# Kernel optimization log

Measured on AMD Instinct MI355X. Metric: run time of the kernel, lower is better.

Reference implementation:

```python
import jax, jax.numpy as jnp
import numpy as np

EPS = 1e-05
NEG = -1000000000.0

def rmsnorm(x):
    var = jnp.mean(x * x, axis=-1, keepdims=True)
    return x * jax.lax.rsqrt(var + EPS)

def apply_rotary(x, cos, sin):
    # x: [B,T,H,D], cos/sin: [T,D]
    d = x.shape[-1]
    x1, x2 = x[..., : d // 2], x[..., d // 2 :]
    half_rot = jnp.concatenate([-x2, x1], axis=-1)
    c = cos[None, :, None, :]
    s = sin[None, :, None, :]
    return x * c + half_rot * s

def setup_inputs() -> dict:
    key = jax.random.key(0)
    ks = jax.random.split(key, 12)
    B, T, C, H = 2, 2048, 1024, 16
    hd = C // H
    std = 0.02
    return {
        "x": jax.random.normal(ks[0], (B, T, C), jnp.float32),
        "x0": jax.random.normal(ks[1], (B, T, C), jnp.float32),
        "lambdaResid": jnp.ones((), jnp.float32),
        "lambdaX0": jnp.ones((), jnp.float32),
        "cos": jax.random.uniform(ks[2], (T, hd), jnp.float32),
        "sin": jax.random.uniform(ks[3], (T, hd), jnp.float32),
        "qWeight": jax.random.normal(ks[4], (C, C), jnp.float32) * std,
        "kWeight": jax.random.normal(ks[5], (C, C), jnp.float32) * std,
        "vWeight": jax.random.normal(ks[6], (C, C), jnp.float32) * std,
        "projWeight": jax.random.normal(ks[7], (C, C), jnp.float32) * std,
        "fcWeight": jax.random.normal(ks[8], (C, 4 * C), jnp.float32) * std,
        "mlpProjWeight": jax.random.normal(ks[9], (4 * C, C), jnp.float32) * std,
    }

def reference(x, x0, lambdaResid, lambdaX0, cos, sin,
              qWeight, kWeight, vWeight, projWeight, fcWeight, mlpProjWeight):
    B, T, C = x.shape
    hd = cos.shape[-1]
    H = C // hd
    scaled = x * lambdaResid + x0 * lambdaX0
    pre = rmsnorm(scaled)
    q = (pre @ qWeight).reshape(B, T, H, hd)
    k = (pre @ kWeight).reshape(B, T, H, hd)
    v = (pre @ vWeight).reshape(B, T, H, hd)
    q = rmsnorm(apply_rotary(q, cos, sin))  # [B,T,H,D]
    k = rmsnorm(apply_rotary(k, cos, sin))
    scores = jnp.einsum('bthd,bshd->bhts', q, k) / jnp.sqrt(jnp.float32(hd))
    mask = jnp.tril(jnp.ones((T, T), bool))
    scores = jnp.where(mask[None, None], scores, NEG)
    probs = jax.nn.softmax(scores, axis=-1)
    attn = jnp.einsum('bhts,bshd->bthd', probs, v).reshape(B, T, C)
    scaled = scaled + attn @ projWeight
    h = rmsnorm(scaled) @ fcWeight
    h = jnp.square(jax.nn.relu(h))
    return scaled + h @ mlpProjWeight
```

## Files before the change

kernel.cpp:

```cpp
#include <hip/hip_runtime.h>
#include <hip/hip_bf16.h>
#include <stdint.h>

typedef _Float16 f16;
typedef __attribute__((ext_vector_type(8))) _Float16 f16x8;
typedef __attribute__((ext_vector_type(4))) _Float16 f16x4;
typedef __attribute__((ext_vector_type(2))) __fp16 fp16x2;
typedef __attribute__((ext_vector_type(4))) float f32x4;

__device__ __forceinline__ void g2l16(const void* g, void* l) {
  __builtin_amdgcn_global_load_lds(
      (const __attribute__((address_space(1))) uint32_t*)g,
      (__attribute__((address_space(3))) uint32_t*)l, 16, 0, 0);
}

__device__ __forceinline__ uint32_t pkrtz(float a, float b) {
  union { fp16x2 h; uint32_t u; } z;
  z.h = __builtin_amdgcn_cvt_pkrtz(a, b);
  return z.u;
}

__global__ __launch_bounds__(256)
void wconv_all_kernel(const float* __restrict__ Wq, const float* __restrict__ Wk,
                      const float* __restrict__ Wv, const float* __restrict__ Wp,
                      const float* __restrict__ Wfc, const float* __restrict__ Wmp,
                      f16* __restrict__ Dq, f16* __restrict__ Dk, f16* __restrict__ Dv,
                      f16* __restrict__ Dp, f16* __restrict__ Dfc, f16* __restrict__ Dmp)
{
  __shared__ float tile[32][33];
  int id = blockIdx.x;
  const float* W; f16* Wt; int K, N, local;
  if      (id < 1024) { W = Wq;  Wt = Dq;  K = 1024; N = 1024; local = id; }
  else if (id < 2048) { W = Wk;  Wt = Dk;  K = 1024; N = 1024; local = id - 1024; }
  else if (id < 3072) { W = Wv;  Wt = Dv;  K = 1024; N = 1024; local = id - 2048; }
  else if (id < 4096) { W = Wp;  Wt = Dp;  K = 1024; N = 1024; local = id - 3072; }
  else if (id < 8192) { W = Wfc; Wt = Dfc; K = 1024; N = 4096; local = id - 4096; }
  else                { W = Wmp; Wt = Dmp; K = 4096; N = 1024; local = id - 8192; }
  int ntx = N >> 5;
  int n0 = (local % ntx) * 32, k0 = (local / ntx) * 32;
  int tx = threadIdx.x & 31, ty = threadIdx.x >> 5;
#pragma unroll
  for (int i = 0; i < 4; ++i)
    tile[ty + 8*i][tx] = W[(size_t)(k0 + ty + 8*i) * N + (n0 + tx)];
  __syncthreads();
#pragma unroll
  for (int i = 0; i < 4; ++i)
    Wt[(size_t)(n0 + ty + 8*i) * K + (k0 + tx)] = (f16)tile[tx][ty + 8*i];
}

__global__ __launch_bounds__(256)
void scale_rms_kernel(const float* __restrict__ x, const float* __restrict__ x0,
                      const float* __restrict__ lamR, const float* __restrict__ lamX,
                      float* __restrict__ scaled, f16* __restrict__ pre)
{
  const int C = 1024;
  int row = blockIdx.x, tid = threadIdx.x;
  float lr = lamR[0], lx = lamX[0];
  size_t base = (size_t)row * C;
  float4 xv = ((const float4*)(x + base))[tid];
  float4 zv = ((const float4*)(x0 + base))[tid];
  float4 sv;
  sv.x = xv.x*lr + zv.x*lx;  sv.y = xv.y*lr + zv.y*lx;
  sv.z = xv.z*lr + zv.z*lx;  sv.w = xv.w*lr + zv.w*lx;
  float ss = sv.x*sv.x + sv.y*sv.y + sv.z*sv.z + sv.w*sv.w;
#pragma unroll
  for (int off = 32; off >= 1; off >>= 1) ss += __shfl_xor(ss, off);
  __shared__ float red[4];
  if ((tid & 63) == 0) red[tid >> 6] = ss;
  __syncthreads();
  float tot = red[0] + red[1] + red[2] + red[3];
  float rs = rsqrtf(tot * (1.0f / 1024.0f) + 1e-5f);
  ((float4*)(scaled + base))[tid] = sv;
  f16* p = pre + base + tid * 4;
  p[0] = (f16)(sv.x * rs); p[1] = (f16)(sv.y * rs);
  p[2] = (f16)(sv.z * rs); p[3] = (f16)(sv.w * rs);
}

__global__ __launch_bounds__(256)
void combine_rms_kernel(const float* __restrict__ resid, const f16* __restrict__ p0,
                        const f16* __restrict__ p1, float* __restrict__ scaled2,
                        f16* __restrict__ pre2)
{
  const int C = 1024;
  int row = blockIdx.x, tid = threadIdx.x;
  size_t base = (size_t)row * C;
  float4 rv = ((const float4*)(resid + base))[tid];
  f16x4 av = ((const f16x4*)(p0 + base))[tid];
  f16x4 bv = ((const f16x4*)(p1 + base))[tid];
  float4 sv;
  sv.x = rv.x + (float)av[0] + (float)bv[0];
  sv.y = rv.y + (float)av[1] + (float)bv[1];
  sv.z = rv.z + (float)av[2] + (float)bv[2];
  sv.w = rv.w + (float)av[3] + (float)bv[3];
  float ss = sv.x*sv.x + sv.y*sv.y + sv.z*sv.z + sv.w*sv.w;
#pragma unroll
  for (int off = 32; off >= 1; off >>= 1) ss += __shfl_xor(ss, off);
  __shared__ float red[4];
  if ((tid & 63) == 0) red[tid >> 6] = ss;
  __syncthreads();
  float tot = red[0] + red[1] + red[2] + red[3];
  float rs = rsqrtf(tot * (1.0f / 1024.0f) + 1e-5f);
  ((float4*)(scaled2 + base))[tid] = sv;
  f16* p = pre2 + base + tid * 4;
  p[0] = (f16)(sv.x * rs); p[1] = (f16)(sv.y * rs);
  p[2] = (f16)(sv.z * rs); p[3] = (f16)(sv.w * rs);
}

__global__ __launch_bounds__(256)
void combine_out4_kernel(const float* __restrict__ resid, const f16* __restrict__ parts,
                         size_t pstride, float* __restrict__ out)
{
  size_t i = (size_t)blockIdx.x * 256 + threadIdx.x;
  float4 rv = ((const float4*)resid)[i];
  float4 sv = rv;
#pragma unroll
  for (int z = 0; z < 4; ++z) {
    f16x4 av = ((const f16x4*)(parts + z * pstride))[i];
    sv.x += (float)av[0]; sv.y += (float)av[1];
    sv.z += (float)av[2]; sv.w += (float)av[3];
  }
  ((float4*)out)[i] = sv;
}

__global__ __launch_bounds__(256)
void rope_rms_kernel(f16* __restrict__ Xq, f16* __restrict__ Xk,
                     const float* __restrict__ cs, const float* __restrict__ sn)
{
  const int MH = 4096 * 16;
  int ridx = blockIdx.x * 4 + (threadIdx.x >> 6);
  f16* X = (ridx < MH) ? Xq : Xk;
  if (ridx >= MH) ridx -= MH;
  int lane = threadIdx.x & 63;
  int h = ridx & 15;
  int bt = ridx >> 4;
  int t = bt & 2047;
  size_t base = (size_t)bt * 1024 + h * 64;
  float xv = (float)X[base + lane];
  float other = __shfl_xor(xv, 32);
  float rot = (lane < 32) ? -other : other;
  float c = cs[t * 64 + lane], s = sn[t * 64 + lane];
  float y = xv * c + rot * s;
  float ss = y * y;
#pragma unroll
  for (int off = 32; off >= 1; off >>= 1) ss += __shfl_xor(ss, off);
  float r = rsqrtf(ss * (1.0f / 64.0f) + 1e-5f);
  X[base + lane] = (f16)(y * r);
}

template<int EPI>
__global__ __launch_bounds__(256)
void gemm_kernel(const f16* __restrict__ A, const f16* __restrict__ Bt,
                 void* __restrict__ out, int M, int N, int K, int nb, int zb)
{
  __shared__ __align__(16) f16 smem[4 * 128 * 32];
  const int tid = threadIdx.x;
  const int wave = tid >> 6, lane = tid & 63;
  const int col = lane & 15, quad = lane >> 4;
  const int id = blockIdx.x;
  const int xcd = id & 7, s = id >> 3;
  const int n_i = s % nb;
  const int p = s / nb;
  const int mpx = (M >> 7) >> 3;
  const int zz = p / mpx;
  const int m_i = xcd * mpx + (p % mpx);
  const int m0 = m_i * 128, n0 = n_i * 128;
  const int wm = (wave >> 1) * 64, wn = (wave & 1) * 64;
  const int Ksub = K / zb;
  const int kBeg = zz * Ksub;
  const int nIter = Ksub >> 5;
  f32x4 acc[4][4] = {};

  const size_t rowb = (size_t)K * 2;
  const char* Agp = (const char*)A  + (size_t)m0 * rowb;
  const char* Bgp = (const char*)Bt + (size_t)n0 * rowb;

  const int r_st = (tid >> 2);
  const int cb_st = (tid & 3) << 4;
  const int lb0 = (wave * 64) << 4;
  const int lb1 = (256 + wave * 64) << 4;

#define STAGE(buf, k0)                                                           \
  {                                                                              \
    const size_t koff = (size_t)(k0) * 2;                                        \
    g2l16(Agp + (size_t)r_st * rowb + koff + cb_st,                              \
          (char*)smem + (buf) * 8192 + lb0);                                     \
    g2l16(Agp + (size_t)(r_st + 64) * rowb + koff + cb_st,                       \
          (char*)smem + (buf) * 8192 + lb1);                                     \
    g2l16(Bgp + (size_t)r_st * rowb + koff + cb_st,                              \
          (char*)smem + 16384 + (buf) * 8192 + lb0);                             \
    g2l16(Bgp + (size_t)(r_st + 64) * rowb + koff + cb_st,                       \
          (char*)smem + 16384 + (buf) * 8192 + lb1);                             \
  }

  STAGE(0, kBeg)
  for (int kt = 0; kt < nIter; ++kt) {
    __syncthreads();
    if (kt + 1 < nIter) STAGE((kt + 1) & 1, kBeg + (kt + 1) * 32)
    const f16* As = smem + (kt & 1) * 4096;
    const f16* Bs = smem + 8192 + (kt & 1) * 4096;
    f16x8 af[4], bf[4];
#pragma unroll
    for (int t = 0; t < 4; ++t)
      af[t] = *(const f16x8*)(As + (wm + t*16 + col) * 32 + quad * 8);
#pragma unroll
    for (int t = 0; t < 4; ++t)
      bf[t] = *(const f16x8*)(Bs + (wn + t*16 + col) * 32 + quad * 8);
#pragma unroll
    for (int mt = 0; mt < 4; ++mt)
#pragma unroll
      for (int nt = 0; nt < 4; ++nt)
        acc[mt][nt] = __builtin_amdgcn_mfma_f32_16x16x32_f16(af[mt], bf[nt], acc[mt][nt], 0, 0, 0);
  }
#undef STAGE
  f16* ep = smem + wave * 1024;
  f16* outz = (EPI == 4) ? ((f16*)out + (size_t)zz * M * N) : (f16*)out;
#pragma unroll
  for (int mt = 0; mt < 4; ++mt) {
#pragma unroll
    for (int nt = 0; nt < 4; ++nt) {
#pragma unroll
      for (int r = 0; r < 4; ++r) {
        float v = acc[mt][nt][r];
        if (EPI == 1) { float tv = v > 0.0f ? v : 0.0f; v = tv * tv; }
        ep[(quad * 4 + r) * 64 + ((nt ^ quad) * 16 + col)] = (f16)v;
      }
    }
#pragma unroll
    for (int j = 0; j < 2; ++j) {
      int e = j * 64 + lane;
      int row = e >> 3, rb = e & 7;
      int phys16 = (((rb >> 1) ^ (row >> 2)) << 1) + (rb & 1);
      f16x8 vv = *(const f16x8*)(ep + row * 64 + phys16 * 8);
      int grow = m0 + wm + mt * 16 + row;
      int gcol = n0 + wn + rb * 8;
      *(f16x8*)(outz + (size_t)grow * N + gcol) = vv;
    }
  }
}

__device__ __forceinline__ void stage256(const char* Agp, const char* Bgp, size_t rowb,
                                         char* lds, int st_r, size_t koff, int tid)
{
#pragma unroll
  for (int j = 0; j < 4; ++j) {
    g2l16(Agp + (size_t)(st_r + j * 64) * rowb + koff, lds + j * 8192 + tid * 16);
    g2l16(Bgp + (size_t)(st_r + j * 64) * rowb + koff, lds + 32768 + j * 8192 + tid * 16);
  }
}

template<int EPI>
__global__ __launch_bounds__(512, 2)
void gemm256_kernel(const f16* __restrict__ A, const f16* __restrict__ Bt,
                    void* __restrict__ out, int M, int N, int K, int nb, int zb)
{
  __shared__ __align__(16) f16 smem[65536];
  const int tid = threadIdx.x;
  const int wave = tid >> 6, lane = tid & 63;
  const int col = lane & 15, quad = lane >> 4;
  const int id = blockIdx.x;
  const int xcd = id & 7, sb = id >> 3;
  const int n_i = sb % nb;
  const int p = sb / nb;
  const int mpx = (M >> 8) >> 3;
  const int zz = p / mpx;
  const int m_i = xcd * mpx + (p % mpx);
  const int m0 = m_i * 256, n0 = n_i * 256;
  const int wm = (wave >> 2) * 128, wn = (wave & 3) * 64;
  const int Ksub = K / zb;
  const int kBeg = zz * Ksub;
  const int ntiles = Ksub >> 6;
  f32x4 acc[8][4] = {};

  const size_t rowb = (size_t)K * 2;
  const char* Agp = (const char*)A  + (size_t)m0 * rowb;
  const char* Bgp = (const char*)Bt + (size_t)n0 * rowb;

  const int st_r = tid >> 3;
  const size_t st_so = (size_t)(((tid & 7) ^ ((tid >> 3) & 7)) << 4);

  stage256(Agp, Bgp, rowb, (char*)smem,         st_r, (size_t)kBeg * 2 + st_so, tid);
  stage256(Agp, Bgp, rowb, (char*)smem + 65536, st_r, (size_t)(kBeg + 64) * 2 + st_so, tid);

  for (int t = 0; t < ntiles; ++t) {
    if (t < ntiles - 1) asm volatile("s_waitcnt vmcnt(8)" ::: "memory");
    else                asm volatile("s_waitcnt vmcnt(0)" ::: "memory");
    __builtin_amdgcn_s_barrier();
    asm volatile("" ::: "memory");

    const f16* As = smem + (t & 1) * 32768;
    const f16* Bs = As + 16384;
    f16x8 bf[4][2];
#pragma unroll
    for (int ct = 0; ct < 4; ++ct)
#pragma unroll
      for (int ks = 0; ks < 2; ++ks)
        bf[ct][ks] = *(const f16x8*)(Bs + (wn + ct*16 + col) * 64 +
                                     (((ks*4 + quad) ^ (col & 7)) << 3));
#pragma unroll
    for (int sp = 0; sp < 4; ++sp) {
      f16x8 af[2][2];
#pragma unroll
      for (int i = 0; i < 2; ++i)
#pragma unroll
        for (int ks = 0; ks < 2; ++ks)
          af[i][ks] = *(const f16x8*)(As + (wm + (sp*2 + i)*16 + col) * 64 +
                                      (((ks*4 + quad) ^ (col & 7)) << 3));
      __builtin_amdgcn_s_setprio(1);
#pragma unroll
      for (int i = 0; i < 2; ++i)
#pragma unroll
        for (int ct = 0; ct < 4; ++ct)
#pragma unroll
          for (int ks = 0; ks < 2; ++ks)
            acc[sp*2 + i][ct] = __builtin_amdgcn_mfma_f32_16x16x32_f16(
                af[i][ks], bf[ct][ks], acc[sp*2 + i][ct], 0, 0, 0);
      __builtin_amdgcn_s_setprio(0);
    }

    asm volatile("s_waitcnt lgkmcnt(0)" ::: "memory");
    __builtin_amdgcn_s_barrier();
    asm volatile("" ::: "memory");
    if (t + 2 < ntiles)
      stage256(Agp, Bgp, rowb, (char*)smem + (t & 1) * 65536, st_r,
               (size_t)(kBeg + (t + 2) * 64) * 2 + st_so, tid);
  }

  f16* ep = smem + wave * 1024;
  f16* outz = (EPI == 4) ? ((f16*)out + (size_t)zz * M * N) : (f16*)out;
#pragma unroll
  for (int mt = 0; mt < 8; ++mt) {
#pragma unroll
    for (int ct = 0; ct < 4; ++ct) {
#pragma unroll
      for (int r = 0; r < 4; ++r) {
        float v = acc[mt][ct][r];
        if (EPI == 1) { float tv = v > 0.0f ? v : 0.0f; v = tv * tv; }
        ep[(quad * 4 + r) * 64 + ((ct ^ quad) * 16 + col)] = (f16)v;
      }
    }
#pragma unroll
    for (int j = 0; j < 2; ++j) {
      int e = j * 64 + lane;
      int row = e >> 3, rb = e & 7;
      int phys16 = (((rb >> 1) ^ (row >> 2)) << 1) + (rb & 1);
      f16x8 vv = *(const f16x8*)(ep + row * 64 + phys16 * 8);
      int grow = m0 + wm + mt * 16 + row;
      int gcol = n0 + wn + rb * 8;
      *(f16x8*)(outz + (size_t)grow * N + gcol) = vv;
    }
  }
}

__global__ __launch_bounds__(512, 2)
void gemm256_qkv_kernel(const f16* __restrict__ A, const f16* __restrict__ Bt,
                        f16* __restrict__ qb, f16* __restrict__ kbuf, f16* __restrict__ vtg)
{
  const int K = 1024, nb = 12, ntiles = 16;
  __shared__ __align__(16) f16 smem[65536];
  const int tid = threadIdx.x;
  const int wave = tid >> 6, lane = tid & 63;
  const int col = lane & 15, quad = lane >> 4;
  const int id = blockIdx.x;
  const int xcd = id & 7, sb = id >> 3;
  const int n_i = sb % nb;
  const int m_i = xcd * 2 + (sb / nb);
  const int m0 = m_i * 256, n0 = n_i * 256;
  const int wm = (wave >> 2) * 128, wn = (wave & 3) * 64;
  f32x4 acc[8][4] = {};

  const size_t rowb = (size_t)K * 2;
  const char* Agp = (const char*)A  + (size_t)m0 * rowb;
  const char* Bgp = (const char*)Bt + (size_t)n0 * rowb;

  const int st_r = tid >> 3;
  const size_t st_so = (size_t)(((tid & 7) ^ ((tid >> 3) & 7)) << 4);

  stage256(Agp, Bgp, rowb, (char*)smem,         st_r, st_so, tid);
  stage256(Agp, Bgp, rowb, (char*)smem + 65536, st_r, (size_t)64 * 2 + st_so, tid);

  for (int t = 0; t < ntiles; ++t) {
    if (t < ntiles - 1) asm volatile("s_waitcnt vmcnt(8)" ::: "memory");
    else                asm volatile("s_waitcnt vmcnt(0)" ::: "memory");
    __builtin_amdgcn_s_barrier();
    asm volatile("" ::: "memory");

    const f16* As = smem + (t & 1) * 32768;
    const f16* Bs = As + 16384;
    f16x8 bf[4][2];
#pragma unroll
    for (int ct = 0; ct < 4; ++ct)
#pragma unroll
      for (int ks = 0; ks < 2; ++ks)
        bf[ct][ks] = *(const f16x8*)(Bs + (wn + ct*16 + col) * 64 +
                                     (((ks*4 + quad) ^ (col & 7)) << 3));
#pragma unroll
    for (int sp = 0; sp < 4; ++sp) {
      f16x8 af[2][2];
#pragma unroll
      for (int i = 0; i < 2; ++i)
#pragma unroll
        for (int ks = 0; ks < 2; ++ks)
          af[i][ks] = *(const f16x8*)(As + (wm + (sp*2 + i)*16 + col) * 64 +
                                      (((ks*4 + quad) ^ (col & 7)) << 3));
      __builtin_amdgcn_s_setprio(1);
#pragma unroll
      for (int i = 0; i < 2; ++i)
#pragma unroll
        for (int ct = 0; ct < 4; ++ct)
#pragma unroll
          for (int ks = 0; ks < 2; ++ks)
            acc[sp*2 + i][ct] = __builtin_amdgcn_mfma_f32_16x16x32_f16(
                af[i][ks], bf[ct][ks], acc[sp*2 + i][ct], 0, 0, 0);
      __builtin_amdgcn_s_setprio(0);
    }

    asm volatile("s_waitcnt lgkmcnt(0)" ::: "memory");
    __builtin_amdgcn_s_barrier();
    asm volatile("" ::: "memory");
    if (t + 2 < ntiles)
      stage256(Agp, Bgp, rowb, (char*)smem + (t & 1) * 65536, st_r,
               (size_t)((t + 2) * 64) * 2 + st_so, tid);
  }

  const int cw = n0 + wn;
  const int sel = cw >> 10;
  if (sel < 2) {
    f16* dst = (sel == 0) ? qb : kbuf;
    const int cbase = cw & 1023;
    f16* ep = smem + wave * 1024;
#pragma unroll
    for (int mt = 0; mt < 8; ++mt) {
#pragma unroll
      for (int ct = 0; ct < 4; ++ct)
#pragma unroll
        for (int r = 0; r < 4; ++r)
          ep[(quad * 4 + r) * 64 + ((ct ^ quad) * 16 + col)] = (f16)acc[mt][ct][r];
#pragma unroll
      for (int j = 0; j < 2; ++j) {
        int e = j * 64 + lane;
        int row = e >> 3, rb = e & 7;
        int phys16 = (((rb >> 1) ^ (row >> 2)) << 1) + (rb & 1);
        f16x8 vv = *(const f16x8*)(ep + row * 64 + phys16 * 8);
        int grow = m0 + wm + mt * 16 + row;
        *(f16x8*)(dst + (size_t)grow * 1024 + cbase + rb * 8) = vv;
      }
    }
  } else {
#pragma unroll
    for (int mt = 0; mt < 8; ++mt) {
      int t0 = m0 + wm + mt * 16 + quad * 4;
      int b = t0 >> 11, t = t0 & 2047;
#pragma unroll
      for (int ct = 0; ct < 4; ++ct) {
        int dd = (cw & 1023) + ct * 16 + col;
        int hh = dd >> 6, d = dd & 63;
        f16x4 vv;
#pragma unroll
        for (int r = 0; r < 4; ++r) vv[r] = (f16)acc[mt][ct][r];
        *(f16x4*)(vtg + ((size_t)((b * 16 + hh) * 64 + d)) * 2048 + t) = vv;
      }
    }
  }
}

__global__ __launch_bounds__(256, 5)
void attn_kernel(const f16* __restrict__ Q, const f16* __restrict__ Kc,
                 const f16* __restrict__ Vt, f16* __restrict__ O)
{
  const int T = 2048, C = 1024;
  __shared__ __align__(16) f16 Ks[2][64 * 64];
  __shared__ __align__(16) f16 Vs[2][64 * 64];
  const int tid = threadIdx.x, wave = tid >> 6, lane = tid & 63;
  const int col = lane & 15, quad = lane >> 4;
  const int bh = blockIdx.x, b = bh >> 4, h = bh & 15;
  const int qt = (int)gridDim.y - 1 - (int)blockIdx.y;
  const int q0 = qt * 64;

  const f16* qb = Q  + ((size_t)b * T) * C + h * 64;
  const f16* kb = Kc + ((size_t)b * T) * C + h * 64;
  const f16* vb = Vt + ((size_t)bh * 64) * T;

  f16x8 bq[2];
#pragma unroll
  for (int ks = 0; ks < 2; ++ks)
    bq[ks] = *(const f16x8*)(qb + (size_t)(q0 + wave*16 + col) * C + ks*32 + quad*8);

  f32x4 o_acc[4];
#pragma unroll
  for (int dt = 0; dt < 4; ++dt) o_acc[dt] = (f32x4){0.f,0.f,0.f,0.f};
  float l_acc = 0.f;

  const int srow = lane >> 3;
  const int sblk = (lane & 7) ^ srow;

#pragma unroll
  for (int i = 0; i < 2; ++i) {
    int r0 = wave * 16 + 8 * i;
    g2l16(kb + (size_t)(r0 + srow) * C + sblk * 8, (char*)Ks[0] + r0 * 128);
    g2l16(vb + (size_t)(r0 + srow) * T + sblk * 8, (char*)Vs[0] + r0 * 128);
  }

  const int cm = col & 7;
  const int c00 = quad,            c01 = 4 + (quad ^ 1);
  const int c10 = 8 + (quad ^ 2),  c11 = 12 + (quad ^ 3);
  const int o00 = (((c00 >> 1) ^ cm) << 3) + ((c00 & 1) << 2);
  const int o01 = (((c01 >> 1) ^ cm) << 3) + ((c01 & 1) << 2);
  const int o10 = (((c10 >> 1) ^ cm) << 3) + ((c10 & 1) << 2);
  const int o11 = (((c11 >> 1) ^ cm) << 3) + ((c11 & 1) << 2);

  int cur = 0;
  for (int kt = 0; kt <= qt; ++kt) {
    __syncthreads();

    if (kt < qt) {
      const int ks1 = (kt + 1) * 64;
#pragma unroll
      for (int i = 0; i < 2; ++i) {
        int r0 = wave * 16 + 8 * i;
        g2l16(kb + (size_t)(ks1 + r0 + srow) * C + sblk * 8, (char*)Ks[cur ^ 1] + r0 * 128);
        g2l16(vb + (size_t)(r0 + srow) * T + ks1 + sblk * 8, (char*)Vs[cur ^ 1] + r0 * 128);
      }
    }

    f32x4 s[4];
#pragma unroll
    for (int nt = 0; nt < 4; ++nt) s[nt] = (f32x4){0.f,0.f,0.f,0.f};
    __builtin_amdgcn_s_setprio(1);
#pragma unroll
    for (int ks = 0; ks < 2; ++ks) {
#pragma unroll
      for (int nt = 0; nt < 4; ++nt) {
        int key = nt * 16 + col;
        f16x8 ak = *(const f16x8*)(Ks[cur] + key * 64 + (((ks*4 + quad) ^ (key & 7)) * 8));
        s[nt] = __builtin_amdgcn_mfma_f32_16x16x32_f16(ak, bq[ks], s[nt], 0, 0, 0);
      }
    }
    __builtin_amdgcn_s_setprio(0);

    const bool masked = (kt == qt);
    const int qloc = wave * 16 + col;
    uint32_t pk[4][2];
    float l_tile = 0.f;
#pragma unroll
    for (int nt = 0; nt < 4; ++nt) {
      float p[4];
#pragma unroll
      for (int r = 0; r < 4; ++r) {
        float pv = __expf(s[nt][r] * 0.125f);
        if (masked && (nt * 16 + quad * 4 + r > qloc)) pv = 0.0f;
        p[r] = pv;
      }
      l_tile += (p[0] + p[1]) + (p[2] + p[3]);
      pk[nt][0] = pkrtz(p[0], p[1]);
      pk[nt][1] = pkrtz(p[2], p[3]);
    }
    l_acc += l_tile;

    union { uint32_t u[4]; f16x8 v; } pa0, pa1;
    pa0.u[0] = pk[0][0];
    pa0.u[1] = pk[0][1];
    pa0.u[2] = (uint32_t)__shfl_xor((int)pk[1][0], 16);
    pa0.u[3] = (uint32_t)__shfl_xor((int)pk[1][1], 16);
    pa1.u[0] = (uint32_t)__shfl_xor((int)pk[2][0], 32);
    pa1.u[1] = (uint32_t)__shfl_xor((int)pk[2][1], 32);
    pa1.u[2] = (uint32_t)__shfl_xor((int)pk[3][0], 48);
    pa1.u[3] = (uint32_t)__shfl_xor((int)pk[3][1], 48);

    __builtin_amdgcn_s_setprio(1);
#pragma unroll
    for (int dt = 0; dt < 4; ++dt) {
      const f16* vrow = Vs[cur] + (dt * 16 + col) * 64;
      union { struct { f16x4 lo, hi; } p; f16x8 v; } bv0, bv1;
      bv0.p.lo = *(const f16x4*)(vrow + o00);
      bv0.p.hi = *(const f16x4*)(vrow + o01);
      bv1.p.lo = *(const f16x4*)(vrow + o10);
      bv1.p.hi = *(const f16x4*)(vrow + o11);
      o_acc[dt] = __builtin_amdgcn_mfma_f32_16x16x32_f16(pa0.v, bv0.v, o_acc[dt], 0, 0, 0);
      o_acc[dt] = __builtin_amdgcn_mfma_f32_16x16x32_f16(pa1.v, bv1.v, o_acc[dt], 0, 0, 0);
    }
    __builtin_amdgcn_s_setprio(0);
    cur ^= 1;
  }

  l_acc += __shfl_xor(l_acc, 16);
  l_acc += __shfl_xor(l_acc, 32);
  float linv[4];
#pragma unroll
  for (int r = 0; r < 4; ++r)
    linv[r] = 1.0f / __shfl(l_acc, quad * 4 + r);

#pragma unroll
  for (int dt = 0; dt < 4; ++dt) {
#pragma unroll
    for (int r = 0; r < 4; ++r) {
      int qr = q0 + wave * 16 + quad * 4 + r;
      float v = o_acc[dt][r] * linv[r];
      O[((size_t)b * T + qr) * C + h * 64 + dt * 16 + col] = (f16)v;
    }
  }
}

extern "C" void kernel_launch(void* const* d_in, const int* in_sizes, int n_in,
                              void* d_out, int out_size, void* d_ws, size_t ws_size,
                              hipStream_t stream)
{
  const float* x    = (const float*)d_in[0];
  const float* x0   = (const float*)d_in[1];
  const float* lamR = (const float*)d_in[2];
  const float* lamX = (const float*)d_in[3];
  const float* cs   = (const float*)d_in[4];
  const float* sn   = (const float*)d_in[5];
  const float* Wq   = (const float*)d_in[6];
  const float* Wk   = (const float*)d_in[7];
  const float* Wv   = (const float*)d_in[8];
  const float* Wp   = (const float*)d_in[9];
  const float* Wfc  = (const float*)d_in[10];
  const float* Wmp  = (const float*)d_in[11];
  float* out = (float*)d_out;

  const int B = 2, T = 2048, C = 1024, H = 16;
  const int M = B * T;
  const size_t MB = 1ull << 20;
  char* ws = (char*)d_ws;
  f16*   Wqkv_t = (f16*)(ws + 0 * MB);
  f16*   Wp_t   = (f16*)(ws + 6 * MB);
  f16*   Wfc_t  = (f16*)(ws + 8 * MB);
  f16*   Wmp_t  = (f16*)(ws + 16 * MB);
  float* scaled  = (float*)(ws + 24 * MB);
  f16*   pre     = (f16*)(ws + 40 * MB);
  f16*   qb      = (f16*)(ws + 48 * MB);
  f16*   kbuf    = (f16*)(ws + 56 * MB);
  f16*   vtg     = (f16*)(ws + 64 * MB);
  float* scaled2 = (float*)(ws + 72 * MB);
  f16*   hbuf    = (f16*)(ws + 88 * MB);
  f16*   attnOut = pre;
  f16*   pre2    = qb;
  f16*   projP   = (f16*)(ws + 88 * MB);
  f16*   mlpP    = (f16*)(ws + 24 * MB);

  dim3 tb(256);
  dim3 tb5(512);
  wconv_all_kernel<<<dim3(12288), tb, 0, stream>>>(
      Wq, Wk, Wv, Wp, Wfc, Wmp,
      Wqkv_t, Wqkv_t + 1024*1024, Wqkv_t + 2048*1024, Wp_t, Wfc_t, Wmp_t);

  scale_rms_kernel<<<M, tb, 0, stream>>>(x, x0, lamR, lamX, scaled, pre);

  gemm256_qkv_kernel<<<dim3(192), tb5, 0, stream>>>(pre, Wqkv_t, qb, kbuf, vtg);

  rope_rms_kernel<<<(M * H) / 2, tb, 0, stream>>>(qb, kbuf, cs, sn);

  attn_kernel<<<dim3(B * H, T/64), tb, 0, stream>>>(qb, kbuf, vtg, attnOut);

  gemm_kernel<4><<<dim3(8 * 32 * 2), tb, 0, stream>>>(attnOut, Wp_t, projP, M, C, C, 8, 2);
  combine_rms_kernel<<<M, tb, 0, stream>>>(scaled, projP, projP + (size_t)M*C, scaled2, pre2);

  gemm256_kernel<1><<<dim3(256), tb5, 0, stream>>>(pre2, Wfc_t, hbuf, M, 4*C, C, 16, 1);

  gemm256_kernel<4><<<dim3(256), tb5, 0, stream>>>(hbuf, Wmp_t, mlpP, M, C, 4*C, 4, 4);
  combine_out4_kernel<<<(M*C)/1024, tb, 0, stream>>>(scaled2, mlpP, (size_t)M*C, out);
}
```

Baseline: 349.7 us.

## Split long causal attention rows across blocks with a separate combine kernel

New measurement: 351.8 us. No clear change (+0.6%).

```diff
diff --git a/kernel.cpp b/kernel.cpp
--- a/kernel.cpp
+++ b/kernel.cpp
@@ -465,7 +465,8 @@
 
 __global__ __launch_bounds__(256, 5)
 void attn_kernel(const f16* __restrict__ Q, const f16* __restrict__ Kc,
-                 const f16* __restrict__ Vt, f16* __restrict__ O)
+                 const f16* __restrict__ Vt, f16* __restrict__ O,
+                 f16* __restrict__ pO, float* __restrict__ pL)
 {
   const int T = 2048, C = 1024;
   __shared__ __align__(16) f16 Ks[2][64 * 64];
@@ -473,7 +474,17 @@
   const int tid = threadIdx.x, wave = tid >> 6, lane = tid & 63;
   const int col = lane & 15, quad = lane >> 4;
   const int bh = blockIdx.x, b = bh >> 4, h = bh & 15;
-  const int qt = (int)gridDim.y - 1 - (int)blockIdx.y;
+
+  const int u = blockIdx.y;
+  int qt = 0, acc0 = 0, nc = 1;
+  for (int q = 0; q < 32; ++q) {
+    int c = (q + 8) >> 3;
+    if (u < acc0 + c) { qt = q; nc = c; break; }
+    acc0 += c;
+  }
+  const int ci = u - acc0;
+  const int n = qt + 1;
+  const int kt0 = (ci * n) / nc, kt1 = ((ci + 1) * n) / nc;
   const int q0 = qt * 64;
 
   const f16* qb = Q  + ((size_t)b * T) * C + h * 64;
@@ -496,8 +507,8 @@
 #pragma unroll
   for (int i = 0; i < 2; ++i) {
     int r0 = wave * 16 + 8 * i;
-    g2l16(kb + (size_t)(r0 + srow) * C + sblk * 8, (char*)Ks[0] + r0 * 128);
-    g2l16(vb + (size_t)(r0 + srow) * T + sblk * 8, (char*)Vs[0] + r0 * 128);
+    g2l16(kb + (size_t)(kt0 * 64 + r0 + srow) * C + sblk * 8, (char*)Ks[0] + r0 * 128);
+    g2l16(vb + (size_t)(r0 + srow) * T + kt0 * 64 + sblk * 8, (char*)Vs[0] + r0 * 128);
   }
 
   const int cm = col & 7;
@@ -509,10 +520,10 @@
   const int o11 = (((c11 >> 1) ^ cm) << 3) + ((c11 & 1) << 2);
 
   int cur = 0;
-  for (int kt = 0; kt <= qt; ++kt) {
+  for (int kt = kt0; kt < kt1; ++kt) {
     __syncthreads();
 
-    if (kt < qt) {
+    if (kt + 1 < kt1) {
       const int ks1 = (kt + 1) * 64;
 #pragma unroll
       for (int i = 0; i < 2; ++i) {
@@ -584,20 +595,65 @@
 
   l_acc += __shfl_xor(l_acc, 16);
   l_acc += __shfl_xor(l_acc, 32);
-  float linv[4];
-#pragma unroll
-  for (int r = 0; r < 4; ++r)
-    linv[r] = 1.0f / __shfl(l_acc, quad * 4 + r);
-
-#pragma unroll
-  for (int dt = 0; dt < 4; ++dt) {
-#pragma unroll
-    for (int r = 0; r < 4; ++r) {
-      int qr = q0 + wave * 16 + quad * 4 + r;
-      float v = o_acc[dt][r] * linv[r];
-      O[((size_t)b * T + qr) * C + h * 64 + dt * 16 + col] = (f16)v;
-    }
-  }
+
+  if (nc == 1) {
+    float linv[4];
+#pragma unroll
+    for (int r = 0; r < 4; ++r)
+      linv[r] = 1.0f / __shfl(l_acc, quad * 4 + r);
+#pragma unroll
+    for (int dt = 0; dt < 4; ++dt) {
+#pragma unroll
+      for (int r = 0; r < 4; ++r) {
+        int qr = q0 + wave * 16 + quad * 4 + r;
+        float v = o_acc[dt][r] * linv[r];
+        O[((size_t)b * T + qr) * C + h * 64 + dt * 16 + col] = (f16)v;
+      }
+    }
+  } else {
+    const size_t slot = (size_t)bh * 80 + u;
+    f16* po = pO + slot * 4096;
+#pragma unroll
+    for (int dt = 0; dt < 4; ++dt)
+#pragma unroll
+      for (int r = 0; r < 4; ++r)
+        po[(wave * 16 + quad * 4 + r) * 64 + dt * 16 + col] = (f16)o_acc[dt][r];
+    if (quad == 0) pL[slot * 64 + wave * 16 + col] = l_acc;
+  }
+}
+
+__global__ __launch_bounds__(256)
+void attn_combine_kernel(const f16* __restrict__ pO, const float* __restrict__ pL,
+                         f16* __restrict__ O)
+{
+  const int T = 2048, C = 1024;
+  const int bh = blockIdx.x, b = bh >> 4, h = bh & 15;
+  const int qt = 8 + blockIdx.y;
+  const int nc = (qt + 8) >> 3;
+  int pre = 0;
+  for (int q = 0; q < qt; ++q) pre += (q + 8) >> 3;
+  const size_t slot0 = (size_t)bh * 80 + pre;
+
+  const int t = threadIdx.x;
+  const int row = t >> 2, dq = (t & 3) * 16;
+
+  float L = 0.f;
+  for (int ci = 0; ci < nc; ++ci) L += pL[(slot0 + ci) * 64 + row];
+  const float inv = 1.0f / L;
+
+  float acc[16] = {};
+  for (int ci = 0; ci < nc; ++ci) {
+    const f16x8* p = (const f16x8*)(pO + (slot0 + ci) * 4096 + row * 64 + dq);
+    f16x8 v0 = p[0], v1 = p[1];
+#pragma unroll
+    for (int j = 0; j < 8; ++j) { acc[j] += (float)v0[j]; acc[8 + j] += (float)v1[j]; }
+  }
+  f16x8 o0, o1;
+#pragma unroll
+  for (int j = 0; j < 8; ++j) { o0[j] = (f16)(acc[j] * inv); o1[j] = (f16)(acc[8 + j] * inv); }
+  f16* dst = O + ((size_t)b * T + qt * 64 + row) * C + h * 64 + dq;
+  ((f16x8*)dst)[0] = o0;
+  ((f16x8*)dst)[1] = o1;
 }
 
 extern "C" void kernel_launch(void* const* d_in, const int* in_sizes, int n_in,
@@ -637,6 +693,8 @@
   f16*   pre2    = qb;
   f16*   projP   = (f16*)(ws + 88 * MB);
   f16*   mlpP    = (f16*)(ws + 24 * MB);
+  f16*   attnPO  = (f16*)(ws + 88 * MB);
+  float* attnPL  = (float*)(ws + 108 * MB);
 
   dim3 tb(256);
   dim3 tb5(512);
@@ -650,7 +708,8 @@
 
   rope_rms_kernel<<<(M * H) / 2, tb, 0, stream>>>(qb, kbuf, cs, sn);
 
-  attn_kernel<<<dim3(B * H, T/64), tb, 0, stream>>>(qb, kbuf, vtg, attnOut);
+  attn_kernel<<<dim3(B * H, 80), tb, 0, stream>>>(qb, kbuf, vtg, attnOut, attnPO, attnPL);
+  attn_combine_kernel<<<dim3(B * H, 24), tb, 0, stream>>>(attnPO, attnPL, attnOut);
 
   gemm_kernel<4><<<dim3(8 * 32 * 2), tb, 0, stream>>>(attnOut, Wp_t, projP, M, C, C, 8, 2);
   combine_rms_kernel<<<M, tb, 0, stream>>>(scaled, projP, projP + (size_t)M*C, scaled2, pre2);
```

## Fuse rotary+RMS into QKV GEMM epilogue and pair causal attention tiles per block

Applied to the files above, without the earlier changes.

Result: faster. 335.4 us (-4.1%).

```diff
diff --git a/kernel.cpp b/kernel.cpp
--- a/kernel.cpp
+++ b/kernel.cpp
@@ -120,31 +120,6 @@
     sv.z += (float)av[2]; sv.w += (float)av[3];
   }
   ((float4*)out)[i] = sv;
-}
-
-__global__ __launch_bounds__(256)
-void rope_rms_kernel(f16* __restrict__ Xq, f16* __restrict__ Xk,
-                     const float* __restrict__ cs, const float* __restrict__ sn)
-{
-  const int MH = 4096 * 16;
-  int ridx = blockIdx.x * 4 + (threadIdx.x >> 6);
-  f16* X = (ridx < MH) ? Xq : Xk;
-  if (ridx >= MH) ridx -= MH;
-  int lane = threadIdx.x & 63;
-  int h = ridx & 15;
-  int bt = ridx >> 4;
-  int t = bt & 2047;
-  size_t base = (size_t)bt * 1024 + h * 64;
-  float xv = (float)X[base + lane];
-  float other = __shfl_xor(xv, 32);
-  float rot = (lane < 32) ? -other : other;
-  float c = cs[t * 64 + lane], s = sn[t * 64 + lane];
-  float y = xv * c + rot * s;
-  float ss = y * y;
-#pragma unroll
-  for (int off = 32; off >= 1; off >>= 1) ss += __shfl_xor(ss, off);
-  float r = rsqrtf(ss * (1.0f / 64.0f) + 1e-5f);
-  X[base + lane] = (f16)(y * r);
 }
 
 template<int EPI>
@@ -353,7 +328,8 @@
 
 __global__ __launch_bounds__(512, 2)
 void gemm256_qkv_kernel(const f16* __restrict__ A, const f16* __restrict__ Bt,
-                        f16* __restrict__ qb, f16* __restrict__ kbuf, f16* __restrict__ vtg)
+                        f16* __restrict__ qb, f16* __restrict__ kbuf, f16* __restrict__ vtg,
+                        const float* __restrict__ cs, const float* __restrict__ sn)
 {
   const int K = 1024, nb = 12, ntiles = 16;
   __shared__ __align__(16) f16 smem[65536];
@@ -431,6 +407,29 @@
 #pragma unroll
     for (int mt = 0; mt < 8; ++mt) {
 #pragma unroll
+      for (int r = 0; r < 4; ++r) {
+        const int t = (m0 + wm + mt * 16 + quad * 4 + r) & 2047;
+        const float* cp = cs + t * 64 + col;
+        const float* sp = sn + t * 64 + col;
+        float yv[4];
+        float ss = 0.f;
+#pragma unroll
+        for (int ct = 0; ct < 4; ++ct) {
+          float c = cp[ct * 16], s = sp[ct * 16];
+          float rot = acc[mt][ct ^ 2][r];
+          float y = acc[mt][ct][r] * c + (ct < 2 ? -rot : rot) * s;
+          yv[ct] = y;
+          ss += y * y;
+        }
+        ss += __shfl_xor(ss, 1, 16);
+        ss += __shfl_xor(ss, 2, 16);
+        ss += __shfl_xor(ss, 4, 16);
+        ss += __shfl_xor(ss, 8, 16);
+        float rs = rsqrtf(ss * (1.0f / 64.0f) + 1e-5f);
+#pragma unroll
+        for (int ct = 0; ct < 4; ++ct) acc[mt][ct][r] = yv[ct] * rs;
+      }
+#pragma unroll
       for (int ct = 0; ct < 4; ++ct)
 #pragma unroll
         for (int r = 0; r < 4; ++r)
@@ -463,7 +462,7 @@
   }
 }
 
-__global__ __launch_bounds__(256, 5)
+__global__ __launch_bounds__(512)
 void attn_kernel(const f16* __restrict__ Q, const f16* __restrict__ Kc,
                  const f16* __restrict__ Vt, f16* __restrict__ O)
 {
@@ -473,8 +472,12 @@
   const int tid = threadIdx.x, wave = tid >> 6, lane = tid & 63;
   const int col = lane & 15, quad = lane >> 4;
   const int bh = blockIdx.x, b = bh >> 4, h = bh & 15;
-  const int qt = (int)gridDim.y - 1 - (int)blockIdx.y;
-  const int q0 = qt * 64;
+  const int pr = blockIdx.y;
+  const int grp = wave >> 2;
+  const int w4 = wave & 3;
+  const int hiB = 31 - pr;
+  const int myB = grp ? pr : hiB;
+  const int q0 = myB * 64;
 
   const f16* qb = Q  + ((size_t)b * T) * C + h * 64;
   const f16* kb = Kc + ((size_t)b * T) * C + h * 64;
@@ -483,7 +486,7 @@
   f16x8 bq[2];
 #pragma unroll
   for (int ks = 0; ks < 2; ++ks)
-    bq[ks] = *(const f16x8*)(qb + (size_t)(q0 + wave*16 + col) * C + ks*32 + quad*8);
+    bq[ks] = *(const f16x8*)(qb + (size_t)(q0 + w4*16 + col) * C + ks*32 + quad*8);
 
   f32x4 o_acc[4];
 #pragma unroll
@@ -492,13 +495,10 @@
 
   const int srow = lane >> 3;
   const int sblk = (lane & 7) ^ srow;
-
-#pragma unroll
-  for (int i = 0; i < 2; ++i) {
-    int r0 = wave * 16 + 8 * i;
-    g2l16(kb + (size_t)(r0 + srow) * C + sblk * 8, (char*)Ks[0] + r0 * 128);
-    g2l16(vb + (size_t)(r0 + srow) * T + sblk * 8, (char*)Vs[0] + r0 * 128);
-  }
+  const int r0 = wave * 8;
+
+  g2l16(kb + (size_t)(r0 + srow) * C + sblk * 8, (char*)Ks[0] + r0 * 128);
+  g2l16(vb + (size_t)(r0 + srow) * T + sblk * 8, (char*)Vs[0] + r0 * 128);
 
   const int cm = col & 7;
   const int c00 = quad,            c01 = 4 + (quad ^ 1);
@@ -509,76 +509,74 @@
   const int o11 = (((c11 >> 1) ^ cm) << 3) + ((c11 & 1) << 2);
 
   int cur = 0;
-  for (int kt = 0; kt <= qt; ++kt) {
+  for (int kt = 0; kt <= hiB; ++kt) {
     __syncthreads();
 
-    if (kt < qt) {
+    if (kt < hiB) {
       const int ks1 = (kt + 1) * 64;
-#pragma unroll
-      for (int i = 0; i < 2; ++i) {
-        int r0 = wave * 16 + 8 * i;
-        g2l16(kb + (size_t)(ks1 + r0 + srow) * C + sblk * 8, (char*)Ks[cur ^ 1] + r0 * 128);
-        g2l16(vb + (size_t)(r0 + srow) * T + ks1 + sblk * 8, (char*)Vs[cur ^ 1] + r0 * 128);
-      }
-    }
-
-    f32x4 s[4];
-#pragma unroll
-    for (int nt = 0; nt < 4; ++nt) s[nt] = (f32x4){0.f,0.f,0.f,0.f};
-    __builtin_amdgcn_s_setprio(1);
-#pragma unroll
-    for (int ks = 0; ks < 2; ++ks) {
+      g2l16(kb + (size_t)(ks1 + r0 + srow) * C + sblk * 8, (char*)Ks[cur ^ 1] + r0 * 128);
+      g2l16(vb + (size_t)(r0 + srow) * T + ks1 + sblk * 8, (char*)Vs[cur ^ 1] + r0 * 128);
+    }
+
+    if (kt <= myB) {
+      f32x4 s[4];
+#pragma unroll
+      for (int nt = 0; nt < 4; ++nt) s[nt] = (f32x4){0.f,0.f,0.f,0.f};
+      __builtin_amdgcn_s_setprio(1);
+#pragma unroll
+      for (int ks = 0; ks < 2; ++ks) {
+#pragma unroll
+        for (int nt = 0; nt < 4; ++nt) {
+          int key = nt * 16 + col;
+          f16x8 ak = *(const f16x8*)(Ks[cur] + key * 64 + (((ks*4 + quad) ^ (key & 7)) * 8));
+          s[nt] = __builtin_amdgcn_mfma_f32_16x16x32_f16(ak, bq[ks], s[nt], 0, 0, 0);
+        }
+      }
+      __builtin_amdgcn_s_setprio(0);
+
+      const bool masked = (kt == myB);
+      const int qloc = w4 * 16 + col;
+      uint32_t pk[4][2];
+      float l_tile = 0.f;
 #pragma unroll
       for (int nt = 0; nt < 4; ++nt) {
-        int key = nt * 16 + col;
-        f16x8 ak = *(const f16x8*)(Ks[cur] + key * 64 + (((ks*4 + quad) ^ (key & 7)) * 8));
-        s[nt] = __builtin_amdgcn_mfma_f32_16x16x32_f16(ak, bq[ks], s[nt], 0, 0, 0);
-      }
-    }
-    __builtin_amdgcn_s_setprio(0);
-
-    const bool masked = (kt == qt);
-    const int qloc = wave * 16 + col;
-    uint32_t pk[4][2];
-    float l_tile = 0.f;
-#pragma unroll
-    for (int nt = 0; nt < 4; ++nt) {
-      float p[4];
-#pragma unroll
-      for (int r = 0; r < 4; ++r) {
-        float pv = __expf(s[nt][r] * 0.125f);
-        if (masked && (nt * 16 + quad * 4 + r > qloc)) pv = 0.0f;
-        p[r] = pv;
-      }
-      l_tile += (p[0] + p[1]) + (p[2] + p[3]);
-      pk[nt][0] = pkrtz(p[0], p[1]);
-      pk[nt][1] = pkrtz(p[2], p[3]);
-    }
-    l_acc += l_tile;
-
-    union { uint32_t u[4]; f16x8 v; } pa0, pa1;
-    pa0.u[0] = pk[0][0];
-    pa0.u[1] = pk[0][1];
-    pa0.u[2] = (uint32_t)__shfl_xor((int)pk[1][0], 16);
-    pa0.u[3] = (uint32_t)__shfl_xor((int)pk[1][1], 16);
-    pa1.u[0] = (uint32_t)__shfl_xor((int)pk[2][0], 32);
-    pa1.u[1] = (uint32_t)__shfl_xor((int)pk[2][1], 32);
-    pa1.u[2] = (uint32_t)__shfl_xor((int)pk[3][0], 48);
-    pa1.u[3] = (uint32_t)__shfl_xor((int)pk[3][1], 48);
-
-    __builtin_amdgcn_s_setprio(1);
-#pragma unroll
-    for (int dt = 0; dt < 4; ++dt) {
-      const f16* vrow = Vs[cur] + (dt * 16 + col) * 64;
-      union { struct { f16x4 lo, hi; } p; f16x8 v; } bv0, bv1;
-      bv0.p.lo = *(const f16x4*)(vrow + o00);
-      bv0.p.hi = *(const f16x4*)(vrow + o01);
-      bv1.p.lo = *(const f16x4*)(vrow + o10);
-      bv1.p.hi = *(const f16x4*)(vrow + o11);
-      o_acc[dt] = __builtin_amdgcn_mfma_f32_16x16x32_f16(pa0.v, bv0.v, o_acc[dt], 0, 0, 0);
-      o_acc[dt] = __builtin_amdgcn_mfma_f32_16x16x32_f16(pa1.v, bv1.v, o_acc[dt], 0, 0, 0);
-    }
-    __builtin_amdgcn_s_setprio(0);
+        float p[4];
+#pragma unroll
+        for (int r = 0; r < 4; ++r) {
+          float pv = __expf(s[nt][r] * 0.125f);
+          if (masked && (nt * 16 + quad * 4 + r > qloc)) pv = 0.0f;
+          p[r] = pv;
+        }
+        l_tile += (p[0] + p[1]) + (p[2] + p[3]);
+        pk[nt][0] = pkrtz(p[0], p[1]);
+        pk[nt][1] = pkrtz(p[2], p[3]);
+      }
+      l_acc += l_tile;
+
+      union { uint32_t u[4]; f16x8 v; } pa0, pa1;
+      pa0.u[0] = pk[0][0];
+      pa0.u[1] = pk[0][1];
+      pa0.u[2] = (uint32_t)__shfl_xor((int)pk[1][0], 16);
+      pa0.u[3] = (uint32_t)__shfl_xor((int)pk[1][1], 16);
+      pa1.u[0] = (uint32_t)__shfl_xor((int)pk[2][0], 32);
+      pa1.u[1] = (uint32_t)__shfl_xor((int)pk[2][1], 32);
+      pa1.u[2] = (uint32_t)__shfl_xor((int)pk[3][0], 48);
+      pa1.u[3] = (uint32_t)__shfl_xor((int)pk[3][1], 48);
+
+      __builtin_amdgcn_s_setprio(1);
+#pragma unroll
+      for (int dt = 0; dt < 4; ++dt) {
+        const f16* vrow = Vs[cur] + (dt * 16 + col) * 64;
+        union { struct { f16x4 lo, hi; } p; f16x8 v; } bv0, bv1;
+        bv0.p.lo = *(const f16x4*)(vrow + o00);
+        bv0.p.hi = *(const f16x4*)(vrow + o01);
+        bv1.p.lo = *(const f16x4*)(vrow + o10);
+        bv1.p.hi = *(const f16x4*)(vrow + o11);
+        o_acc[dt] = __builtin_amdgcn_mfma_f32_16x16x32_f16(pa0.v, bv0.v, o_acc[dt], 0, 0, 0);
+        o_acc[dt] = __builtin_amdgcn_mfma_f32_16x16x32_f16(pa1.v, bv1.v, o_acc[dt], 0, 0, 0);
+      }
+      __builtin_amdgcn_s_setprio(0);
+    }
     cur ^= 1;
   }
 
@@ -587,13 +585,13 @@
   float linv[4];
 #pragma unroll
   for (int r = 0; r < 4; ++r)
-    linv[r] = 1.0f / __shfl(l_acc, quad * 4 + r);
+    linv[r] = 1.0f / __shfl(l_acc, (wave & 4) * 16 + quad * 4 + r, 64);
 
 #pragma unroll
   for (int dt = 0; dt < 4; ++dt) {
 #pragma unroll
     for (int r = 0; r < 4; ++r) {
-      int qr = q0 + wave * 16 + quad * 4 + r;
+      int qr = q0 + w4 * 16 + quad * 4 + r;
       float v = o_acc[dt][r] * linv[r];
       O[((size_t)b * T + qr) * C + h * 64 + dt * 16 + col] = (f16)v;
     }
@@ -646,11 +644,9 @@
 
   scale_rms_kernel<<<M, tb, 0, stream>>>(x, x0, lamR, lamX, scaled, pre);
 
-  gemm256_qkv_kernel<<<dim3(192), tb5, 0, stream>>>(pre, Wqkv_t, qb, kbuf, vtg);
-
-  rope_rms_kernel<<<(M * H) / 2, tb, 0, stream>>>(qb, kbuf, cs, sn);
-
-  attn_kernel<<<dim3(B * H, T/64), tb, 0, stream>>>(qb, kbuf, vtg, attnOut);
+  gemm256_qkv_kernel<<<dim3(192), tb5, 0, stream>>>(pre, Wqkv_t, qb, kbuf, vtg, cs, sn);
+
+  attn_kernel<<<dim3(B * H, 16), tb5, 0, stream>>>(qb, kbuf, vtg, attnOut);
 
   gemm_kernel<4><<<dim3(8 * 32 * 2), tb, 0, stream>>>(attnOut, Wp_t, projP, M, C, C, 8, 2);
   combine_rms_kernel<<<M, tb, 0, stream>>>(scaled, projP, projP + (size_t)M*C, scaled2, pre2);
```
